# Kernel optimization log

Hardware: AMD Instinct MI355X
Metric: run time of the kernel (lower is better)

Reference implementation:

```python
import jax, jax.numpy as jnp
import numpy as np

B, V, R, P = 1, 2, 512, 64          # batch, views, rays, samples
H, W, F = 480, 640, 256             # image size, feature channels
NEAR, FAR = 0.7, 1.5
DIN = 3 + 3 + (3 + F)               # cam_point(3) + cam_dir(3) + sampled img(3)+feat(F)


def setup_inputs() -> dict:
    key = jax.random.key(0)
    ks = jax.random.split(key, 8)
    ray_origins = jax.random.normal(ks[0], (B, R, 3)) * 0.05
    d = jax.random.normal(ks[1], (B, R, 3)) * 0.2
    d = d.at[..., 2].set(1.0)                      # forward-facing rays (+z)
    ray_directions = d / jnp.linalg.norm(d, axis=-1, keepdims=True)
    images = jax.random.uniform(ks[2], (B, V, H, W, 3))
    K = jnp.array([[500., 0., 320., 0.],
                   [0., 500., 240., 0.],
                   [0., 0., 1., 0.],
                   [0., 0., 0., 1.]])
    intrinsics = jnp.broadcast_to(K, (B, V, 4, 4))
    E = jnp.stack([jnp.eye(4).at[0, 3].set(0.05 * v) for v in range(V)])  # small per-view baseline
    extrinsics_inv = jnp.broadcast_to(E, (B, V, 4, 4))
    combined_features = jax.random.normal(ks[3], (B, V, H, W, F)) * 0.1
    W1 = jax.random.normal(ks[4], (DIN, 128)) * 0.05
    b1 = jnp.zeros((128,))
    W2 = jax.random.normal(ks[5], (128, 128)) * 0.05
    b2 = jnp.zeros((128,))
    Wr = jax.random.normal(ks[6], (128, 4)) * 0.05
    br = jnp.zeros((4,))
    return dict(ray_origins=ray_origins, ray_directions=ray_directions, images=images,
                intrinsics=intrinsics, extrinsics_inv=extrinsics_inv,
                combined_features=combined_features,
                W1=W1, b1=b1, W2=W2, b2=b2, Wr=Wr, br=br)


def bilinear_sample(grid, xy):
    # grid: (B,V,H,W,C), xy: (B,V,R,P,2) pixel coords (x,y) -> (B,V,R,P,C)
    Hh, Ww = grid.shape[2], grid.shape[3]
    x = jnp.clip(xy[..., 0], 0.0, Ww - 1.0)
    y = jnp.clip(xy[..., 1], 0.0, Hh - 1.0)
    x0 = jnp.floor(x).astype(jnp.int32)
    y0 = jnp.floor(y).astype(jnp.int32)
    x1 = jnp.minimum(x0 + 1, Ww - 1)
    y1 = jnp.minimum(y0 + 1, Hh - 1)
    wx = (x - x0)[..., None]
    wy = (y - y0)[..., None]
    bi = jnp.arange(grid.shape[0])[:, None, None, None]
    vi = jnp.arange(grid.shape[1])[None, :, None, None]
    g = lambda yy, xx: grid[bi, vi, yy, xx]
    return (g(y0, x0) * (1 - wx) * (1 - wy) + g(y0, x1) * wx * (1 - wy)
            + g(y1, x0) * (1 - wx) * wy + g(y1, x1) * wx * wy)


def volumetric_render(zs, density, chroma):
    # zs,density: (B,R,P), chroma: (B,R,P,3)
    dists = zs[..., 1:] - zs[..., :-1]
    dists = jnp.concatenate([dists, dists[..., -1:]], axis=-1)
    alpha = 1.0 - jnp.exp(-density * dists)            # sigma_to_alpha
    t = jnp.cumprod(1.0 - alpha + 1e-10, axis=-1)
    trans = jnp.concatenate([jnp.ones_like(t[..., :1]), t[..., :-1]], axis=-1)  # exclusive cumprod
    weights = alpha * trans
    rgb = jnp.sum(weights[..., None] * chroma, axis=-2)
    depth = jnp.sum(weights * zs, axis=-1)
    return rgb, depth, weights


def reference(ray_origins, ray_directions, images, intrinsics, extrinsics_inv,
              combined_features, W1, b1, W2, b2, Wr, br):
    # sample_along_ray
    zs = jnp.broadcast_to(jnp.linspace(NEAR, FAR, P, dtype=jnp.float32), (B, R, P))
    world = ray_origins[:, :, None, :] + zs[..., None] * ray_directions[:, :, None, :]  # (B,R,P,3)
    world_h = jnp.concatenate([world, jnp.ones_like(world[..., :1])], axis=-1)
    # compute_pixel_in_image_mv
    cam = jnp.einsum('bvij,brpj->bvrpi', extrinsics_inv, world_h)          # (B,V,R,P,4)
    pix = jnp.einsum('bvij,bvrpj->bvrpi', intrinsics, cam)
    xy = pix[..., :2] / (pix[..., 2:3] + 1e-8)
    # get_projection_features_mv: gather normalized image + features jointly
    grid = jnp.concatenate([images * 2.0 - 1.0, combined_features], axis=-1)  # (B,V,H,W,3+F)
    feats = bilinear_sample(grid, xy)                                         # (B,V,R,P,3+F)
    # world_to_camera_direction_vector_mv
    cam_dirs = jnp.einsum('bvij,brj->bvri', extrinsics_inv[..., :3, :3], ray_directions)
    dirs = jnp.broadcast_to(cam_dirs[:, :, :, None, :], (B, V, R, P, 3))
    # embedding MLP (MVResNetMLPNeRFEmbedding surrogate) + RenderReadout(4)
    x = jnp.concatenate([cam[..., :3], dirs, feats], axis=-1)                 # (B,V,R,P,DIN)
    h = jax.nn.relu(jnp.einsum('bvrpd,df->bvrpf', x, W1) + b1)
    h = jax.nn.relu(jnp.einsum('bvrpd,df->bvrpf', h, W2) + b2)
    h = h.mean(axis=1)                                                        # fuse views -> (B,R,P,128)
    out = jnp.einsum('brpd,df->brpf', h, Wr) + br
    chroma = jax.nn.sigmoid(out[..., :3])
    density = jax.nn.relu(out[..., 3])
    rgb, depth, _ = volumetric_render(zs, density, chroma)
    return rgb, depth
```

## Files before the change

kernel.cpp:

```cpp
#include <hip/hip_runtime.h>
#include <math.h>

#define NRAYS 512
#define NSAMP 64
#define IMH 480
#define IMW 640
#define NFEAT 256
#define ZNEAR 0.7f
#define ZFAR 1.5f
#define KU1 288
#define W1LO 36864
#define W2OF 73728
#define W2LO 16384
#define H1S 132
#define STGS 36
#define WROW 40
#define WPLANE 5120
#define WBUF 10240

typedef __attribute__((ext_vector_type(8))) short bf16x8;
typedef __attribute__((ext_vector_type(4))) float f32x4;

__device__ __forceinline__ unsigned short bf16rne(float f) {
    unsigned int u = __builtin_bit_cast(unsigned int, f);
    unsigned int r = (u + 0x7FFFu + ((u >> 16) & 1u)) >> 16;
    return (unsigned short)r;
}
__device__ __forceinline__ float bf16tof(unsigned short h) {
    unsigned int u = ((unsigned int)h) << 16;
    return __builtin_bit_cast(float, u);
}
__device__ __forceinline__ unsigned int packsplit(float v) {
    const unsigned short h = bf16rne(v);
    const unsigned short l = bf16rne(v - bf16tof(h));
    return (((unsigned int)h) << 16) | (unsigned int)l;
}
__device__ __forceinline__ void unpack8(uint4 a, uint4 b, bf16x8& hi, bf16x8& lo) {
    union { bf16x8 v; unsigned short u[8]; } H, L;
    const unsigned int w[8] = {a.x, a.y, a.z, a.w, b.x, b.y, b.z, b.w};
    #pragma unroll
    for (int i = 0; i < 8; ++i) {
        H.u[i] = (unsigned short)(w[i] >> 16);
        L.u[i] = (unsigned short)(w[i] & 0xFFFFu);
    }
    hi = H.v; lo = L.v;
}

__global__ __launch_bounds__(256)
void nerf_prep(const float* __restrict__ W1, const float* __restrict__ W2,
               unsigned short* __restrict__ wsu) {
    const int i = blockIdx.x * 256 + threadIdx.x;
    if (i < 36864) {
        const int n = i / KU1, k = i % KU1;
        float val = 0.0f;
        if (k < 9) val = W1[k * 128 + n];
        else if (k >= 16 && k < 272) val = W1[(k - 7) * 128 + n];
        const unsigned short h = bf16rne(val);
        wsu[n * KU1 + k] = h;
        wsu[W1LO + n * KU1 + k] = bf16rne(val - bf16tof(h));
    } else if (i < 53248) {
        const int j = i - 36864;
        const int n = j >> 7, k = j & 127;
        const float val = W2[k * 128 + n];
        const unsigned short h = bf16rne(val);
        wsu[W2OF + n * 128 + k] = h;
        wsu[W2OF + W2LO + n * 128 + k] = bf16rne(val - bf16tof(h));
    }
}

__global__ __launch_bounds__(512, 2)
void nerf_main(const float* __restrict__ rayo,
               const float* __restrict__ rayd,
               const float* __restrict__ images,
               const float* __restrict__ intr,
               const float* __restrict__ einv,
               const float* __restrict__ feats,
               const float* __restrict__ b1,
               const float* __restrict__ b2,
               const float* __restrict__ Wr,
               const float* __restrict__ br,
               const unsigned short* __restrict__ wsu,
               float* __restrict__ out) {
    __shared__ float s_meta[2][NSAMP][12];
    __shared__ float s_cdir[2][4];
    __shared__ unsigned int h1p[2 * NSAMP * H1S];
    __shared__ float s_part[2][NSAMP][4];
    __shared__ unsigned short ldsW[2 * WBUF];

    const int t = threadIdx.x;
    const int r = blockIdx.x;
    const int w8 = __builtin_amdgcn_readfirstlane(t >> 6);
    const int v = w8 >> 2;
    const int wid = w8 & 3;
    const int lane = t & 63;
    const int l15 = lane & 15;
    const int lg  = lane >> 4;
    const int sq  = lane >> 2;
    const int qq  = lane & 3;
    constexpr float STEP = (ZFAR - ZNEAR) / (NSAMP - 1);

    const int sp = t >> 8;
    const int sn = (t & 255) >> 1;
    const int sh = (t & 1) * 16;

    uint4 wa = *reinterpret_cast<const uint4*>(wsu + sp*W1LO + sn*KU1 + sh);
    uint4 wb = *reinterpret_cast<const uint4*>(wsu + sp*W1LO + sn*KU1 + sh + 8);

    if (t < 128) {
        const int vv = t >> 6, p = t & 63;
        const float ox = rayo[r*3+0], oy = rayo[r*3+1], oz = rayo[r*3+2];
        const float dx = rayd[r*3+0], dy = rayd[r*3+1], dz = rayd[r*3+2];
        const float z = ZNEAR + p * STEP;
        const float wxp = ox + z*dx, wyp = oy + z*dy, wzp = oz + z*dz;
        const float* E = einv + vv*16;
        const float cx = E[0]*wxp + E[1]*wyp + E[2]*wzp + E[3];
        const float cy = E[4]*wxp + E[5]*wyp + E[6]*wzp + E[7];
        const float cz = E[8]*wxp + E[9]*wyp + E[10]*wzp + E[11];
        const float cw = E[12]*wxp + E[13]*wyp + E[14]*wzp + E[15];
        const float* Km = intr + vv*16;
        const float px = Km[0]*cx + Km[1]*cy + Km[2]*cz + Km[3]*cw;
        const float py = Km[4]*cx + Km[5]*cy + Km[6]*cz + Km[7]*cw;
        const float pz = Km[8]*cx + Km[9]*cy + Km[10]*cz + Km[11]*cw;
        const float inv = pz + 1e-8f;
        float fx = px / inv, fy = py / inv;
        fx = fminf(fmaxf(fx, 0.0f), (float)(IMW-1));
        fy = fminf(fmaxf(fy, 0.0f), (float)(IMH-1));
        const int x0 = (int)floorf(fx), y0 = (int)floorf(fy);
        const int x1 = min(x0+1, IMW-1), y1 = min(y0+1, IMH-1);
        const int base = vv*IMH*IMW;
        int4 o4; o4.x = (base + y0*IMW + x0) * NFEAT;
                 o4.y = (base + y0*IMW + x1) * NFEAT;
                 o4.z = (base + y1*IMW + x0) * NFEAT;
                 o4.w = (base + y1*IMW + x1) * NFEAT;
        *(int4*)&s_meta[vv][p][0] = o4;
        s_meta[vv][p][4] = fx - (float)x0;
        s_meta[vv][p][5] = fy - (float)y0;
        s_meta[vv][p][6] = cx; s_meta[vv][p][7] = cy; s_meta[vv][p][8] = cz;
        if (p == 0) {
            s_cdir[vv][0] = E[0]*dx + E[1]*dy + E[2]*dz;
            s_cdir[vv][1] = E[4]*dx + E[5]*dy + E[6]*dz;
            s_cdir[vv][2] = E[8]*dx + E[9]*dy + E[10]*dz;
        }
    }
    {
        unsigned short* d = ldsW + sp*WPLANE + sn*WROW + sh;
        *reinterpret_cast<uint4*>(d)     = wa;
        *reinterpret_cast<uint4*>(d + 8) = wb;
    }
    __syncthreads();

    const float* mg = s_meta[v][wid*16 + sq];
    const int4 og = *(const int4*)mg;
    const float wx = mg[4], wy = mg[5];
    const float w00 = (1.f-wx)*(1.f-wy), w01 = wx*(1.f-wy);
    const float w10 = (1.f-wx)*wy,       w11 = wx*wy;
    const float* t00 = feats + og.x;
    const float* t01 = feats + og.y;
    const float* t10 = feats + og.z;
    const float* t11 = feats + og.w;

    float ia = 0.f, ib = 0.f;
    if (qq == 1 || qq == 2) {
        const int i00 = (og.x >> 8) * 3, i01 = (og.y >> 8) * 3;
        const int i10 = (og.z >> 8) * 3, i11 = (og.w >> 8) * 3;
        if (qq == 1) {
            ia = 2.0f*(w00*images[i00+0] + w01*images[i01+0] + w10*images[i10+0] + w11*images[i11+0]) - 1.0f;
            ib = 2.0f*(w00*images[i00+1] + w01*images[i01+1] + w10*images[i10+1] + w11*images[i11+1]) - 1.0f;
        } else {
            ia = 2.0f*(w00*images[i00+2] + w01*images[i01+2] + w10*images[i10+2] + w11*images[i11+2]) - 1.0f;
        }
    }

    unsigned int* stg = h1p + w8 * (16 * H1S);

    f32x4 acc[8];
    #pragma unroll
    for (int nt = 0; nt < 8; ++nt) acc[nt] = f32x4{0.f, 0.f, 0.f, 0.f};

    float4 La[4], Lb[4];
    {
        const int f1 = qq*4;
        Lb[0] = *reinterpret_cast<const float4*>(t00 + f1);
        Lb[1] = *reinterpret_cast<const float4*>(t01 + f1);
        Lb[2] = *reinterpret_cast<const float4*>(t10 + f1);
        Lb[3] = *reinterpret_cast<const float4*>(t11 + f1);
    }
    int cur = 0;
    #pragma unroll
    for (int kc = 0; kc < 9; ++kc) {
        {
            const unsigned short* s = (kc < 8)
                ? (wsu + sp*W1LO + sn*KU1 + (kc+1)*32 + sh)
                : (wsu + W2OF + sp*W2LO + sn*128 + sh);
            wa = *reinterpret_cast<const uint4*>(s);
            wb = *reinterpret_cast<const uint4*>(s + 8);
        }
        float f0[4], f1[4];
        if (kc == 0) {
            if (qq == 0)      { f0[0]=mg[6]; f0[1]=mg[7]; f0[2]=mg[8]; f0[3]=s_cdir[v][0]; }
            else if (qq == 1) { f0[0]=s_cdir[v][1]; f0[1]=s_cdir[v][2]; f0[2]=ia; f0[3]=ib; }
            else if (qq == 2) { f0[0]=ia; f0[1]=0.f; f0[2]=0.f; f0[3]=0.f; }
            else              { f0[0]=0.f; f0[1]=0.f; f0[2]=0.f; f0[3]=0.f; }
        } else {
            f0[0] = w00*La[0].x + w01*La[1].x + w10*La[2].x + w11*La[3].x;
            f0[1] = w00*La[0].y + w01*La[1].y + w10*La[2].y + w11*La[3].y;
            f0[2] = w00*La[0].z + w01*La[1].z + w10*La[2].z + w11*La[3].z;
            f0[3] = w00*La[0].w + w01*La[1].w + w10*La[2].w + w11*La[3].w;
        }
        if (kc == 8) {
            f1[0]=0.f; f1[1]=0.f; f1[2]=0.f; f1[3]=0.f;
        } else {
            f1[0] = w00*Lb[0].x + w01*Lb[1].x + w10*Lb[2].x + w11*Lb[3].x;
            f1[1] = w00*Lb[0].y + w01*Lb[1].y + w10*Lb[2].y + w11*Lb[3].y;
            f1[2] = w00*Lb[0].z + w01*Lb[1].z + w10*Lb[2].z + w11*Lb[3].z;
            f1[3] = w00*Lb[0].w + w01*Lb[1].w + w10*Lb[2].w + w11*Lb[3].w;
        }
        uint4 u0, u1;
        u0.x = packsplit(f0[0]); u0.y = packsplit(f0[1]);
        u0.z = packsplit(f0[2]); u0.w = packsplit(f0[3]);
        u1.x = packsplit(f1[0]); u1.y = packsplit(f1[1]);
        u1.z = packsplit(f1[2]); u1.w = packsplit(f1[3]);
        *reinterpret_cast<uint4*>(stg + sq*STGS + qq*4)      = u0;
        *reinterpret_cast<uint4*>(stg + sq*STGS + 16 + qq*4) = u1;
        const uint4 ua = *reinterpret_cast<const uint4*>(stg + l15*STGS + lg*8);
        const uint4 ub = *reinterpret_cast<const uint4*>(stg + l15*STGS + lg*8 + 4);
        if (kc < 8) {
            const int n0 = (kc+1)*32 + qq*4 - 16;
            La[0] = *reinterpret_cast<const float4*>(t00 + n0);
            La[1] = *reinterpret_cast<const float4*>(t01 + n0);
            La[2] = *reinterpret_cast<const float4*>(t10 + n0);
            La[3] = *reinterpret_cast<const float4*>(t11 + n0);
            if (kc < 7) {
                const int n1 = n0 + 16;
                Lb[0] = *reinterpret_cast<const float4*>(t00 + n1);
                Lb[1] = *reinterpret_cast<const float4*>(t01 + n1);
                Lb[2] = *reinterpret_cast<const float4*>(t10 + n1);
                Lb[3] = *reinterpret_cast<const float4*>(t11 + n1);
            }
        }
        bf16x8 ah, al;
        unpack8(ua, ub, ah, al);
        {
            const unsigned short* wL = ldsW + cur*WBUF + l15*WROW + lg*8;
            #pragma unroll
            for (int nt = 0; nt < 8; ++nt) {
                const bf16x8 bh = *(const bf16x8*)(wL + nt*16*WROW);
                const bf16x8 bl = *(const bf16x8*)(wL + WPLANE + nt*16*WROW);
                acc[nt] = __builtin_amdgcn_mfma_f32_16x16x32_bf16(ah, bh, acc[nt], 0, 0, 0);
                acc[nt] = __builtin_amdgcn_mfma_f32_16x16x32_bf16(al, bh, acc[nt], 0, 0, 0);
                acc[nt] = __builtin_amdgcn_mfma_f32_16x16x32_bf16(ah, bl, acc[nt], 0, 0, 0);
            }
        }
        {
            unsigned short* d = ldsW + (cur^1)*WBUF + sp*WPLANE + sn*WROW + sh;
            *reinterpret_cast<uint4*>(d)     = wa;
            *reinterpret_cast<uint4*>(d + 8) = wb;
        }
        __syncthreads();
        cur ^= 1;
    }

    const int hrow0 = v*NSAMP + wid*16;
    const int hrbase = wid*16 + lg*4;
    #pragma unroll
    for (int nt = 0; nt < 8; ++nt) {
        const int ch = nt * 16 + l15;
        const float bb = b1[ch];
        #pragma unroll
        for (int j = 0; j < 4; ++j) {
            const float hv = fmaxf(acc[nt][j] + bb, 0.0f);
            h1p[(hrow0 + lg*4 + j) * H1S + ch] = packsplit(hv);
        }
    }

    const unsigned int* h1row = h1p + (hrow0 + l15) * H1S;
    #pragma unroll
    for (int nt = 0; nt < 8; ++nt) acc[nt] = f32x4{0.f, 0.f, 0.f, 0.f};
    #pragma unroll
    for (int kc = 0; kc < 4; ++kc) {
        if (kc < 3) {
            const unsigned short* s = wsu + W2OF + sp*W2LO + sn*128 + (kc+1)*32 + sh;
            wa = *reinterpret_cast<const uint4*>(s);
            wb = *reinterpret_cast<const uint4*>(s + 8);
        }
        const uint4 ua = *reinterpret_cast<const uint4*>(h1row + kc*32 + lg*8);
        const uint4 ub = *reinterpret_cast<const uint4*>(h1row + kc*32 + lg*8 + 4);
        bf16x8 a2h, a2l;
        unpack8(ua, ub, a2h, a2l);
        {
            const unsigned short* wL = ldsW + cur*WBUF + l15*WROW + lg*8;
            #pragma unroll
            for (int nt = 0; nt < 8; ++nt) {
                const bf16x8 bh = *(const bf16x8*)(wL + nt*16*WROW);
                const bf16x8 bl = *(const bf16x8*)(wL + WPLANE + nt*16*WROW);
                acc[nt] = __builtin_amdgcn_mfma_f32_16x16x32_bf16(a2h, bh, acc[nt], 0, 0, 0);
                acc[nt] = __builtin_amdgcn_mfma_f32_16x16x32_bf16(a2l, bh, acc[nt], 0, 0, 0);
                acc[nt] = __builtin_amdgcn_mfma_f32_16x16x32_bf16(a2h, bl, acc[nt], 0, 0, 0);
            }
        }
        if (kc < 3) {
            unsigned short* d = ldsW + (cur^1)*WBUF + sp*WPLANE + sn*WROW + sh;
            *reinterpret_cast<uint4*>(d)     = wa;
            *reinterpret_cast<uint4*>(d + 8) = wb;
            __syncthreads();
            cur ^= 1;
        }
    }

    float pr[4][4];
    #pragma unroll
    for (int j = 0; j < 4; ++j)
        #pragma unroll
        for (int q = 0; q < 4; ++q) pr[j][q] = 0.0f;
    #pragma unroll
    for (int nt = 0; nt < 8; ++nt) {
        const int ch = nt * 16 + l15;
        const float bb = b2[ch];
        const float4 wr = *reinterpret_cast<const float4*>(Wr + ch * 4);
        #pragma unroll
        for (int j = 0; j < 4; ++j) {
            const float hv = fmaxf(acc[nt][j] + bb, 0.0f);
            pr[j][0] = fmaf(hv, wr.x, pr[j][0]);
            pr[j][1] = fmaf(hv, wr.y, pr[j][1]);
            pr[j][2] = fmaf(hv, wr.z, pr[j][2]);
            pr[j][3] = fmaf(hv, wr.w, pr[j][3]);
        }
    }
    #pragma unroll
    for (int m = 1; m <= 8; m <<= 1)
        #pragma unroll
        for (int j = 0; j < 4; ++j)
            #pragma unroll
            for (int q = 0; q < 4; ++q)
                pr[j][q] += __shfl_xor(pr[j][q], m, 64);
    if (l15 == 0) {
        #pragma unroll
        for (int j = 0; j < 4; ++j) {
            float4 o;
            o.x = pr[j][0]; o.y = pr[j][1]; o.z = pr[j][2]; o.w = pr[j][3];
            *reinterpret_cast<float4*>(&s_part[v][hrbase + j][0]) = o;
        }
    }
    __syncthreads();

    if (t < NSAMP) {
        const int p = t;
        const float o0 = 0.5f*(s_part[0][p][0] + s_part[1][p][0]) + br[0];
        const float o1 = 0.5f*(s_part[0][p][1] + s_part[1][p][1]) + br[1];
        const float o2 = 0.5f*(s_part[0][p][2] + s_part[1][p][2]) + br[2];
        const float o3 = 0.5f*(s_part[0][p][3] + s_part[1][p][3]) + br[3];
        const float c0 = 1.0f/(1.0f + __expf(-o0));
        const float c1 = 1.0f/(1.0f + __expf(-o1));
        const float c2 = 1.0f/(1.0f + __expf(-o2));
        const float dens = fmaxf(o3, 0.0f);
        const float zp = ZNEAR + p * STEP;
        const float zn = ZNEAR + (p+1) * STEP;
        const float dlast = (ZNEAR + 63*STEP) - (ZNEAR + 62*STEP);
        const float dist = (p == NSAMP-1) ? dlast : (zn - zp);
        const float alpha = 1.0f - __expf(-dens*dist);
        float scan = 1.0f - alpha + 1e-10f;
        #pragma unroll
        for (int off = 1; off < 64; off <<= 1) {
            const float vsh = __shfl_up(scan, off, 64);
            if (p >= off) scan *= vsh;
        }
        float trans = __shfl_up(scan, 1, 64);
        if (p == 0) trans = 1.0f;
        const float w = alpha * trans;
        float s0 = w*c0, s1 = w*c1, s2 = w*c2, sd = w*zp;
        #pragma unroll
        for (int m = 32; m > 0; m >>= 1) {
            s0 += __shfl_xor(s0, m, 64);
            s1 += __shfl_xor(s1, m, 64);
            s2 += __shfl_xor(s2, m, 64);
            sd += __shfl_xor(sd, m, 64);
        }
        if (p == 0) {
            out[r*3+0] = s0; out[r*3+1] = s1; out[r*3+2] = s2;
            out[NRAYS*3 + r] = sd;
        }
    }
}

extern "C" void kernel_launch(void* const* d_in, const int* in_sizes, int n_in,
                              void* d_out, int out_size, void* d_ws, size_t ws_size,
                              hipStream_t stream) {
    const float* rayo   = (const float*)d_in[0];
    const float* rayd   = (const float*)d_in[1];
    const float* images = (const float*)d_in[2];
    const float* intr   = (const float*)d_in[3];
    const float* einv   = (const float*)d_in[4];
    const float* feats  = (const float*)d_in[5];
    const float* W1     = (const float*)d_in[6];
    const float* b1     = (const float*)d_in[7];
    const float* W2     = (const float*)d_in[8];
    const float* b2     = (const float*)d_in[9];
    const float* Wr     = (const float*)d_in[10];
    const float* br     = (const float*)d_in[11];
    float* out = (float*)d_out;
    unsigned short* wsu = (unsigned short*)d_ws;

    hipLaunchKernelGGL(nerf_prep, dim3(208), dim3(256), 0, stream, W1, W2, wsu);
    hipLaunchKernelGGL(nerf_main, dim3(NRAYS), dim3(512), 0, stream,
                       rayo, rayd, images, intr, einv, feats, b1, b2, Wr, br, wsu, out);
}
```

Baseline: 53.97 us.

## Retile MLP onto 32x32x16 MFMA with shared 32-row input staging

```diff
diff --git a/kernel.cpp b/kernel.cpp
--- a/kernel.cpp
+++ b/kernel.cpp
@@ -19,7 +19,7 @@
 #define WBUF 10240
 
 typedef __attribute__((ext_vector_type(8))) short bf16x8;
-typedef __attribute__((ext_vector_type(4))) float f32x4;
+typedef __attribute__((ext_vector_type(16))) float f32x16;
 
 __device__ __forceinline__ unsigned short bf16rne(float f) {
     unsigned int u = __builtin_bit_cast(unsigned int, f);
@@ -81,30 +81,37 @@
                const float* __restrict__ br,
                const unsigned short* __restrict__ wsu,
                float* __restrict__ out) {
-    __shared__ float s_meta[2][NSAMP][12];
+    __shared__ float s_meta[128][12];
     __shared__ float s_cdir[2][4];
-    __shared__ unsigned int h1p[2 * NSAMP * H1S];
-    __shared__ float s_part[2][NSAMP][4];
+    __shared__ unsigned int h1p[128 * H1S];
     __shared__ unsigned short ldsW[2 * WBUF];
+    __shared__ unsigned int xstg[4][2][32 * STGS];
+    __shared__ float s_part[2][128][4];
 
     const int t = threadIdx.x;
     const int r = blockIdx.x;
     const int w8 = __builtin_amdgcn_readfirstlane(t >> 6);
-    const int v = w8 >> 2;
-    const int wid = w8 & 3;
+    const int mt = w8 >> 1;
+    const int np = w8 & 1;
     const int lane = t & 63;
-    const int l15 = lane & 15;
-    const int lg  = lane >> 4;
-    const int sq  = lane >> 2;
-    const int qq  = lane & 3;
+    const int l31 = lane & 31;
+    const int lh = lane >> 5;
+    const int sq = lane >> 2;
+    const int qq = lane & 3;
+    const int vW = w8 >> 2;
+    const int rit = np * 16 + sq;
     constexpr float STEP = (ZFAR - ZNEAR) / (NSAMP - 1);
 
     const int sp = t >> 8;
     const int sn = (t & 255) >> 1;
     const int sh = (t & 1) * 16;
 
-    uint4 wa = *reinterpret_cast<const uint4*>(wsu + sp*W1LO + sn*KU1 + sh);
-    uint4 wb = *reinterpret_cast<const uint4*>(wsu + sp*W1LO + sn*KU1 + sh + 8);
+    uint4 wa, wb;
+    {
+        const unsigned short* s = wsu + sp*W1LO + sn*KU1 + sh;
+        wa = *reinterpret_cast<const uint4*>(s);
+        wb = *reinterpret_cast<const uint4*>(s + 8);
+    }
 
     if (t < 128) {
         const int vv = t >> 6, p = t & 63;
@@ -132,10 +139,10 @@
                  o4.y = (base + y0*IMW + x1) * NFEAT;
                  o4.z = (base + y1*IMW + x0) * NFEAT;
                  o4.w = (base + y1*IMW + x1) * NFEAT;
-        *(int4*)&s_meta[vv][p][0] = o4;
-        s_meta[vv][p][4] = fx - (float)x0;
-        s_meta[vv][p][5] = fy - (float)y0;
-        s_meta[vv][p][6] = cx; s_meta[vv][p][7] = cy; s_meta[vv][p][8] = cz;
+        *(int4*)&s_meta[t][0] = o4;
+        s_meta[t][4] = fx - (float)x0;
+        s_meta[t][5] = fy - (float)y0;
+        s_meta[t][6] = cx; s_meta[t][7] = cy; s_meta[t][8] = cz;
         if (p == 0) {
             s_cdir[vv][0] = E[0]*dx + E[1]*dy + E[2]*dz;
             s_cdir[vv][1] = E[4]*dx + E[5]*dy + E[6]*dz;
@@ -149,7 +156,7 @@
     }
     __syncthreads();
 
-    const float* mg = s_meta[v][wid*16 + sq];
+    const float* mg = s_meta[w8*16 + sq];
     const int4 og = *(const int4*)mg;
     const float wx = mg[4], wy = mg[5];
     const float w00 = (1.f-wx)*(1.f-wy), w01 = wx*(1.f-wy);
@@ -171,12 +178,6 @@
         }
     }
 
-    unsigned int* stg = h1p + w8 * (16 * H1S);
-
-    f32x4 acc[8];
-    #pragma unroll
-    for (int nt = 0; nt < 8; ++nt) acc[nt] = f32x4{0.f, 0.f, 0.f, 0.f};
-
     float4 La[4], Lb[4];
     {
         const int f1 = qq*4;
@@ -185,6 +186,42 @@
         Lb[2] = *reinterpret_cast<const float4*>(t10 + f1);
         Lb[3] = *reinterpret_cast<const float4*>(t11 + f1);
     }
+    {
+        float f0[4], f1[4];
+        if (qq == 0)      { f0[0]=mg[6]; f0[1]=mg[7]; f0[2]=mg[8]; f0[3]=s_cdir[vW][0]; }
+        else if (qq == 1) { f0[0]=s_cdir[vW][1]; f0[1]=s_cdir[vW][2]; f0[2]=ia; f0[3]=ib; }
+        else if (qq == 2) { f0[0]=ia; f0[1]=0.f; f0[2]=0.f; f0[3]=0.f; }
+        else              { f0[0]=0.f; f0[1]=0.f; f0[2]=0.f; f0[3]=0.f; }
+        f1[0] = w00*Lb[0].x + w01*Lb[1].x + w10*Lb[2].x + w11*Lb[3].x;
+        f1[1] = w00*Lb[0].y + w01*Lb[1].y + w10*Lb[2].y + w11*Lb[3].y;
+        f1[2] = w00*Lb[0].z + w01*Lb[1].z + w10*Lb[2].z + w11*Lb[3].z;
+        f1[3] = w00*Lb[0].w + w01*Lb[1].w + w10*Lb[2].w + w11*Lb[3].w;
+        uint4 u0, u1;
+        u0.x = packsplit(f0[0]); u0.y = packsplit(f0[1]);
+        u0.z = packsplit(f0[2]); u0.w = packsplit(f0[3]);
+        u1.x = packsplit(f1[0]); u1.y = packsplit(f1[1]);
+        u1.z = packsplit(f1[2]); u1.w = packsplit(f1[3]);
+        unsigned int* xw = &xstg[mt][0][rit*STGS];
+        *reinterpret_cast<uint4*>(xw + qq*4)      = u0;
+        *reinterpret_cast<uint4*>(xw + 16 + qq*4) = u1;
+    }
+    {
+        const int n0 = 16 + qq*4, n1 = 32 + qq*4;
+        La[0] = *reinterpret_cast<const float4*>(t00 + n0);
+        La[1] = *reinterpret_cast<const float4*>(t01 + n0);
+        La[2] = *reinterpret_cast<const float4*>(t10 + n0);
+        La[3] = *reinterpret_cast<const float4*>(t11 + n0);
+        Lb[0] = *reinterpret_cast<const float4*>(t00 + n1);
+        Lb[1] = *reinterpret_cast<const float4*>(t01 + n1);
+        Lb[2] = *reinterpret_cast<const float4*>(t10 + n1);
+        Lb[3] = *reinterpret_cast<const float4*>(t11 + n1);
+    }
+    __syncthreads();
+
+    f32x16 acc0, acc1;
+    #pragma unroll
+    for (int i = 0; i < 16; ++i) { acc0[i] = 0.0f; acc1[i] = 0.0f; }
+    const int bn0 = (np*2)*32 + l31;
     int cur = 0;
     #pragma unroll
     for (int kc = 0; kc < 9; ++kc) {
@@ -195,60 +232,69 @@
             wa = *reinterpret_cast<const uint4*>(s);
             wb = *reinterpret_cast<const uint4*>(s + 8);
         }
-        float f0[4], f1[4];
-        if (kc == 0) {
-            if (qq == 0)      { f0[0]=mg[6]; f0[1]=mg[7]; f0[2]=mg[8]; f0[3]=s_cdir[v][0]; }
-            else if (qq == 1) { f0[0]=s_cdir[v][1]; f0[1]=s_cdir[v][2]; f0[2]=ia; f0[3]=ib; }
-            else if (qq == 2) { f0[0]=ia; f0[1]=0.f; f0[2]=0.f; f0[3]=0.f; }
-            else              { f0[0]=0.f; f0[1]=0.f; f0[2]=0.f; f0[3]=0.f; }
-        } else {
+        if (kc < 8) {
+            const int c = kc + 1;
+            float f0[4], f1[4];
             f0[0] = w00*La[0].x + w01*La[1].x + w10*La[2].x + w11*La[3].x;
             f0[1] = w00*La[0].y + w01*La[1].y + w10*La[2].y + w11*La[3].y;
             f0[2] = w00*La[0].z + w01*La[1].z + w10*La[2].z + w11*La[3].z;
             f0[3] = w00*La[0].w + w01*La[1].w + w10*La[2].w + w11*La[3].w;
-        }
-        if (kc == 8) {
-            f1[0]=0.f; f1[1]=0.f; f1[2]=0.f; f1[3]=0.f;
-        } else {
-            f1[0] = w00*Lb[0].x + w01*Lb[1].x + w10*Lb[2].x + w11*Lb[3].x;
-            f1[1] = w00*Lb[0].y + w01*Lb[1].y + w10*Lb[2].y + w11*Lb[3].y;
-            f1[2] = w00*Lb[0].z + w01*Lb[1].z + w10*Lb[2].z + w11*Lb[3].z;
-            f1[3] = w00*Lb[0].w + w01*Lb[1].w + w10*Lb[2].w + w11*Lb[3].w;
-        }
-        uint4 u0, u1;
-        u0.x = packsplit(f0[0]); u0.y = packsplit(f0[1]);
-        u0.z = packsplit(f0[2]); u0.w = packsplit(f0[3]);
-        u1.x = packsplit(f1[0]); u1.y = packsplit(f1[1]);
-        u1.z = packsplit(f1[2]); u1.w = packsplit(f1[3]);
-        *reinterpret_cast<uint4*>(stg + sq*STGS + qq*4)      = u0;
-        *reinterpret_cast<uint4*>(stg + sq*STGS + 16 + qq*4) = u1;
-        const uint4 ua = *reinterpret_cast<const uint4*>(stg + l15*STGS + lg*8);
-        const uint4 ub = *reinterpret_cast<const uint4*>(stg + l15*STGS + lg*8 + 4);
-        if (kc < 8) {
-            const int n0 = (kc+1)*32 + qq*4 - 16;
-            La[0] = *reinterpret_cast<const float4*>(t00 + n0);
-            La[1] = *reinterpret_cast<const float4*>(t01 + n0);
-            La[2] = *reinterpret_cast<const float4*>(t10 + n0);
-            La[3] = *reinterpret_cast<const float4*>(t11 + n0);
+            if (c == 8) {
+                f1[0]=0.f; f1[1]=0.f; f1[2]=0.f; f1[3]=0.f;
+            } else {
+                f1[0] = w00*Lb[0].x + w01*Lb[1].x + w10*Lb[2].x + w11*Lb[3].x;
+                f1[1] = w00*Lb[0].y + w01*Lb[1].y + w10*Lb[2].y + w11*Lb[3].y;
+                f1[2] = w00*Lb[0].z + w01*Lb[1].z + w10*Lb[2].z + w11*Lb[3].z;
+                f1[3] = w00*Lb[0].w + w01*Lb[1].w + w10*Lb[2].w + w11*Lb[3].w;
+            }
+            uint4 u0, u1;
+            u0.x = packsplit(f0[0]); u0.y = packsplit(f0[1]);
+            u0.z = packsplit(f0[2]); u0.w = packsplit(f0[3]);
+            u1.x = packsplit(f1[0]); u1.y = packsplit(f1[1]);
+            u1.z = packsplit(f1[2]); u1.w = packsplit(f1[3]);
+            unsigned int* xw = &xstg[mt][cur^1][rit*STGS];
+            *reinterpret_cast<uint4*>(xw + qq*4)      = u0;
+            *reinterpret_cast<uint4*>(xw + 16 + qq*4) = u1;
             if (kc < 7) {
-                const int n1 = n0 + 16;
-                Lb[0] = *reinterpret_cast<const float4*>(t00 + n1);
-                Lb[1] = *reinterpret_cast<const float4*>(t01 + n1);
-                Lb[2] = *reinterpret_cast<const float4*>(t10 + n1);
-                Lb[3] = *reinterpret_cast<const float4*>(t11 + n1);
-            }
-        }
-        bf16x8 ah, al;
-        unpack8(ua, ub, ah, al);
+                const int n0 = (kc+2)*32 - 16 + qq*4;
+                La[0] = *reinterpret_cast<const float4*>(t00 + n0);
+                La[1] = *reinterpret_cast<const float4*>(t01 + n0);
+                La[2] = *reinterpret_cast<const float4*>(t10 + n0);
+                La[3] = *reinterpret_cast<const float4*>(t11 + n0);
+                if (kc < 6) {
+                    const int n1 = n0 + 16;
+                    Lb[0] = *reinterpret_cast<const float4*>(t00 + n1);
+                    Lb[1] = *reinterpret_cast<const float4*>(t01 + n1);
+                    Lb[2] = *reinterpret_cast<const float4*>(t10 + n1);
+                    Lb[3] = *reinterpret_cast<const float4*>(t11 + n1);
+                }
+            }
+        }
         {
-            const unsigned short* wL = ldsW + cur*WBUF + l15*WROW + lg*8;
+            const unsigned int* xb = &xstg[mt][cur][0];
             #pragma unroll
-            for (int nt = 0; nt < 8; ++nt) {
-                const bf16x8 bh = *(const bf16x8*)(wL + nt*16*WROW);
-                const bf16x8 bl = *(const bf16x8*)(wL + WPLANE + nt*16*WROW);
-                acc[nt] = __builtin_amdgcn_mfma_f32_16x16x32_bf16(ah, bh, acc[nt], 0, 0, 0);
-                acc[nt] = __builtin_amdgcn_mfma_f32_16x16x32_bf16(al, bh, acc[nt], 0, 0, 0);
-                acc[nt] = __builtin_amdgcn_mfma_f32_16x16x32_bf16(ah, bl, acc[nt], 0, 0, 0);
+            for (int ks = 0; ks < 2; ++ks) {
+                const uint4 ua = *reinterpret_cast<const uint4*>(xb + l31*STGS + ks*16 + lh*8);
+                const uint4 ub = *reinterpret_cast<const uint4*>(xb + l31*STGS + ks*16 + lh*8 + 4);
+                bf16x8 ah, al;
+                unpack8(ua, ub, ah, al);
+                const unsigned short* wk = ldsW + cur*WBUF + ks*16 + lh*8;
+                {
+                    const unsigned short* wp = wk + bn0*WROW;
+                    const bf16x8 bh = *(const bf16x8*)(wp);
+                    const bf16x8 bl = *(const bf16x8*)(wp + WPLANE);
+                    acc0 = __builtin_amdgcn_mfma_f32_32x32x16_bf16(ah, bh, acc0, 0, 0, 0);
+                    acc0 = __builtin_amdgcn_mfma_f32_32x32x16_bf16(al, bh, acc0, 0, 0, 0);
+                    acc0 = __builtin_amdgcn_mfma_f32_32x32x16_bf16(ah, bl, acc0, 0, 0, 0);
+                }
+                {
+                    const unsigned short* wp = wk + (bn0 + 32)*WROW;
+                    const bf16x8 bh = *(const bf16x8*)(wp);
+                    const bf16x8 bl = *(const bf16x8*)(wp + WPLANE);
+                    acc1 = __builtin_amdgcn_mfma_f32_32x32x16_bf16(ah, bh, acc1, 0, 0, 0);
+                    acc1 = __builtin_amdgcn_mfma_f32_32x32x16_bf16(al, bh, acc1, 0, 0, 0);
+                    acc1 = __builtin_amdgcn_mfma_f32_32x32x16_bf16(ah, bl, acc1, 0, 0, 0);
+                }
             }
         }
         {
@@ -260,22 +306,19 @@
         cur ^= 1;
     }
 
-    const int hrow0 = v*NSAMP + wid*16;
-    const int hrbase = wid*16 + lg*4;
+    {
+        const float b1v0 = b1[bn0], b1v1 = b1[bn0 + 32];
+        #pragma unroll
+        for (int j = 0; j < 16; ++j) {
+            const int row = mt*32 + (j & 3) + 8*(j >> 2) + 4*lh;
+            h1p[row*H1S + bn0]      = packsplit(fmaxf(acc0[j] + b1v0, 0.0f));
+            h1p[row*H1S + bn0 + 32] = packsplit(fmaxf(acc1[j] + b1v1, 0.0f));
+        }
+    }
+    __syncthreads();
+
     #pragma unroll
-    for (int nt = 0; nt < 8; ++nt) {
-        const int ch = nt * 16 + l15;
-        const float bb = b1[ch];
-        #pragma unroll
-        for (int j = 0; j < 4; ++j) {
-            const float hv = fmaxf(acc[nt][j] + bb, 0.0f);
-            h1p[(hrow0 + lg*4 + j) * H1S + ch] = packsplit(hv);
-        }
-    }
-
-    const unsigned int* h1row = h1p + (hrow0 + l15) * H1S;
-    #pragma unroll
-    for (int nt = 0; nt < 8; ++nt) acc[nt] = f32x4{0.f, 0.f, 0.f, 0.f};
+    for (int i = 0; i < 16; ++i) { acc0[i] = 0.0f; acc1[i] = 0.0f; }
     #pragma unroll
     for (int kc = 0; kc < 4; ++kc) {
         if (kc < 3) {
@@ -283,19 +326,29 @@
             wa = *reinterpret_cast<const uint4*>(s);
             wb = *reinterpret_cast<const uint4*>(s + 8);
         }
-        const uint4 ua = *reinterpret_cast<const uint4*>(h1row + kc*32 + lg*8);
-        const uint4 ub = *reinterpret_cast<const uint4*>(h1row + kc*32 + lg*8 + 4);
-        bf16x8 a2h, a2l;
-        unpack8(ua, ub, a2h, a2l);
-        {
-            const unsigned short* wL = ldsW + cur*WBUF + l15*WROW + lg*8;
-            #pragma unroll
-            for (int nt = 0; nt < 8; ++nt) {
-                const bf16x8 bh = *(const bf16x8*)(wL + nt*16*WROW);
-                const bf16x8 bl = *(const bf16x8*)(wL + WPLANE + nt*16*WROW);
-                acc[nt] = __builtin_amdgcn_mfma_f32_16x16x32_bf16(a2h, bh, acc[nt], 0, 0, 0);
-                acc[nt] = __builtin_amdgcn_mfma_f32_16x16x32_bf16(a2l, bh, acc[nt], 0, 0, 0);
-                acc[nt] = __builtin_amdgcn_mfma_f32_16x16x32_bf16(a2h, bl, acc[nt], 0, 0, 0);
+        const unsigned int* hb = h1p + (mt*32 + l31)*H1S + kc*32;
+        #pragma unroll
+        for (int ks = 0; ks < 2; ++ks) {
+            const uint4 ua = *reinterpret_cast<const uint4*>(hb + ks*16 + lh*8);
+            const uint4 ub = *reinterpret_cast<const uint4*>(hb + ks*16 + lh*8 + 4);
+            bf16x8 ah, al;
+            unpack8(ua, ub, ah, al);
+            const unsigned short* wk = ldsW + cur*WBUF + ks*16 + lh*8;
+            {
+                const unsigned short* wp = wk + bn0*WROW;
+                const bf16x8 bh = *(const bf16x8*)(wp);
+                const bf16x8 bl = *(const bf16x8*)(wp + WPLANE);
+                acc0 = __builtin_amdgcn_mfma_f32_32x32x16_bf16(ah, bh, acc0, 0, 0, 0);
+                acc0 = __builtin_amdgcn_mfma_f32_32x32x16_bf16(al, bh, acc0, 0, 0, 0);
+                acc0 = __builtin_amdgcn_mfma_f32_32x32x16_bf16(ah, bl, acc0, 0, 0, 0);
+            }
+            {
+                const unsigned short* wp = wk + (bn0 + 32)*WROW;
+                const bf16x8 bh = *(const bf16x8*)(wp);
+                const bf16x8 bl = *(const bf16x8*)(wp + WPLANE);
+                acc1 = __builtin_amdgcn_mfma_f32_32x32x16_bf16(ah, bh, acc1, 0, 0, 0);
+                acc1 = __builtin_amdgcn_mfma_f32_32x32x16_bf16(al, bh, acc1, 0, 0, 0);
+                acc1 = __builtin_amdgcn_mfma_f32_32x32x16_bf16(ah, bl, acc1, 0, 0, 0);
             }
         }
         if (kc < 3) {
@@ -307,48 +360,45 @@
         }
     }
 
-    float pr[4][4];
-    #pragma unroll
-    for (int j = 0; j < 4; ++j)
-        #pragma unroll
-        for (int q = 0; q < 4; ++q) pr[j][q] = 0.0f;
-    #pragma unroll
-    for (int nt = 0; nt < 8; ++nt) {
-        const int ch = nt * 16 + l15;
-        const float bb = b2[ch];
-        const float4 wr = *reinterpret_cast<const float4*>(Wr + ch * 4);
-        #pragma unroll
-        for (int j = 0; j < 4; ++j) {
-            const float hv = fmaxf(acc[nt][j] + bb, 0.0f);
-            pr[j][0] = fmaf(hv, wr.x, pr[j][0]);
-            pr[j][1] = fmaf(hv, wr.y, pr[j][1]);
-            pr[j][2] = fmaf(hv, wr.z, pr[j][2]);
-            pr[j][3] = fmaf(hv, wr.w, pr[j][3]);
-        }
-    }
-    #pragma unroll
-    for (int m = 1; m <= 8; m <<= 1)
-        #pragma unroll
-        for (int j = 0; j < 4; ++j)
+    {
+        const float b2v0 = b2[bn0], b2v1 = b2[bn0 + 32];
+        const float4 wr0 = *reinterpret_cast<const float4*>(Wr + bn0*4);
+        const float4 wr1 = *reinterpret_cast<const float4*>(Wr + (bn0+32)*4);
+        float pr[16][4];
+        #pragma unroll
+        for (int j = 0; j < 16; ++j) {
+            const float h0 = fmaxf(acc0[j] + b2v0, 0.0f);
+            const float h1v = fmaxf(acc1[j] + b2v1, 0.0f);
+            pr[j][0] = h0*wr0.x + h1v*wr1.x;
+            pr[j][1] = h0*wr0.y + h1v*wr1.y;
+            pr[j][2] = h0*wr0.z + h1v*wr1.z;
+            pr[j][3] = h0*wr0.w + h1v*wr1.w;
+        }
+        #pragma unroll
+        for (int m = 1; m <= 16; m <<= 1)
             #pragma unroll
-            for (int q = 0; q < 4; ++q)
-                pr[j][q] += __shfl_xor(pr[j][q], m, 64);
-    if (l15 == 0) {
-        #pragma unroll
-        for (int j = 0; j < 4; ++j) {
-            float4 o;
-            o.x = pr[j][0]; o.y = pr[j][1]; o.z = pr[j][2]; o.w = pr[j][3];
-            *reinterpret_cast<float4*>(&s_part[v][hrbase + j][0]) = o;
+            for (int j = 0; j < 16; ++j)
+                #pragma unroll
+                for (int q = 0; q < 4; ++q)
+                    pr[j][q] += __shfl_xor(pr[j][q], m, 64);
+        if (l31 == 0) {
+            #pragma unroll
+            for (int j = 0; j < 16; ++j) {
+                const int row = mt*32 + (j & 3) + 8*(j >> 2) + 4*lh;
+                float4 o;
+                o.x = pr[j][0]; o.y = pr[j][1]; o.z = pr[j][2]; o.w = pr[j][3];
+                *reinterpret_cast<float4*>(&s_part[np][row][0]) = o;
+            }
         }
     }
     __syncthreads();
 
     if (t < NSAMP) {
         const int p = t;
-        const float o0 = 0.5f*(s_part[0][p][0] + s_part[1][p][0]) + br[0];
-        const float o1 = 0.5f*(s_part[0][p][1] + s_part[1][p][1]) + br[1];
-        const float o2 = 0.5f*(s_part[0][p][2] + s_part[1][p][2]) + br[2];
-        const float o3 = 0.5f*(s_part[0][p][3] + s_part[1][p][3]) + br[3];
+        const float o0 = 0.5f*((s_part[0][p][0] + s_part[1][p][0]) + (s_part[0][64+p][0] + s_part[1][64+p][0])) + br[0];
+        const float o1 = 0.5f*((s_part[0][p][1] + s_part[1][p][1]) + (s_part[0][64+p][1] + s_part[1][64+p][1])) + br[1];
+        const float o2 = 0.5f*((s_part[0][p][2] + s_part[1][p][2]) + (s_part[0][64+p][2] + s_part[1][64+p][2])) + br[2];
+        const float o3 = 0.5f*((s_part[0][p][3] + s_part[1][p][3]) + (s_part[0][64+p][3] + s_part[1][64+p][3])) + br[3];
         const float c0 = 1.0f/(1.0f + __expf(-o0));
         const float c1 = 1.0f/(1.0f + __expf(-o1));
         const float c2 = 1.0f/(1.0f + __expf(-o2));
```

Measured after the change: 61.02 us. 13.1% more time.
